# Performance work log

Hardware: AMD Instinct MI355X
Metric: run time of the kernel (lower is better)

## Reference

```python
import jax, jax.numpy as jnp
import numpy as np
from jax import lax

B, C, D, H, W = 2, 64, 16, 16, 16  # n = D*H*W = 4096; conv output length = n-2 = 4094
K = 3  # conv kernel size, dilation=2, padding=1


def setup_inputs() -> dict:
    key = jax.random.key(0)
    k1, k2, k3 = jax.random.split(key, 3)
    x = jax.random.normal(k1, (B, C, D, H, W), dtype=jnp.float32)
    # Conv1d params: weight [out_ch, in_ch, k], bias [out_ch]; PyTorch default init scale
    fan_in = C * K
    bound = 1.0 / np.sqrt(fan_in)
    conv_w = jax.random.uniform(k2, (C, C, K), jnp.float32, -bound, bound)
    conv_b = jax.random.uniform(k3, (C,), jnp.float32, -bound, bound)
    return {"x": x, "conv_w": conv_w, "conv_b": conv_b}


def _dspa(x, conv_w, conv_b):
    b, c, d, h, w = x.shape
    x1 = x.reshape(b, c, -1)  # [b, c, n]
    # dilated Conv1d: kernel=3, stride=1, padding=1, dilation=2 -> length n-2
    x2 = lax.conv_general_dilated(
        x1, conv_w,
        window_strides=(1,), padding=[(1, 1)], rhs_dilation=(2,),
        dimension_numbers=("NCH", "OIH", "NCH"),
    ) + conv_b[None, :, None]  # [b, c, n-2]
    # scores = bmm(x1^T, x2): [b, n, n-2]
    scores = jnp.einsum("bcn,bcm->bnm", x1, x2)
    # torch nn.Softmax() (dim=None) on a 3D tensor resolves to dim=0 (legacy behavior)
    x3 = jax.nn.softmax(scores, axis=0)  # [b, n, n-2]
    # x4 = bmm(x2, x3^T): [b, c, n]
    x4 = jnp.einsum("bcm,bnm->bcn", x2, x3)
    out = x1 + x4
    return out.reshape(b, c, d, h, w)


def reference(x, conv_w, conv_b):
    return _dspa(x, conv_w, conv_b)
```

## Files before the change

### kernel.cpp

```cpp
#include <hip/hip_runtime.h>

typedef unsigned short u16;
typedef unsigned int u32;
typedef __attribute__((ext_vector_type(8))) short bf16x8;
typedef __attribute__((ext_vector_type(4))) float f32x4;

#define NJ 4094

__device__ __forceinline__ u16 f2bf(float f) {
  union { float f; unsigned u; } v;
  v.f = f;
  unsigned r = v.u + 0x7fffu + ((v.u >> 16) & 1u);
  return (u16)(r >> 16);
}

__device__ __forceinline__ u32 pk_bf(float a, float b) {
  u32 ua = __float_as_uint(a) + 0x8000u;
  u32 ub = __float_as_uint(b) + 0x8000u;
  return __builtin_amdgcn_perm(ub, ua, 0x07060302u);
}

__global__ __launch_bounds__(256) void conv_kernel(
    const float* __restrict__ x, const float* __restrict__ w,
    const float* __restrict__ bias, u16* __restrict__ x2n, u16* __restrict__ x2T,
    float* __restrict__ out) {
  __shared__ float xs[64 * 68];
  __shared__ float wl[64 * 64 * 3];
  const int b = blockIdx.x >> 6, jt = blockIdx.x & 63;
  const int t = threadIdx.x;
  for (int idx = t; idx < 64 * 68; idx += 256) {
    int i = idx / 68, p = idx - i * 68;
    int jg = jt * 64 - 1 + p;
    float v = 0.f;
    if (jg >= 0 && jg < 4096) v = x[(b * 64 + i) * 4096 + jg];
    xs[idx] = v;
  }
  for (int idx = t; idx < 64 * 64 * 3; idx += 256) {
    int tap = idx % 3, ci = idx / 3;
    int c = ci >> 6, i = ci & 63;
    wl[(i * 64 + c) * 3 + tap] = w[idx];
  }
  __syncthreads();
  for (int idx = t; idx < 64 * 64; idx += 256) {
    int i = idx >> 6, k = idx & 63;
    out[(b * 64 + i) * 4096 + jt * 64 + k] = xs[i * 68 + k + 1];
  }
  const int c = t & 63, jsub = t >> 6;
  float acc[16];
  float bv = bias[c];
#pragma unroll
  for (int k = 0; k < 16; k++) acc[k] = bv;
  for (int i = 0; i < 64; i++) {
    float w0 = wl[(i * 64 + c) * 3 + 0];
    float w1 = wl[(i * 64 + c) * 3 + 1];
    float w2 = wl[(i * 64 + c) * 3 + 2];
    const float* xr = &xs[i * 68 + jsub * 16];
#pragma unroll
    for (int k = 0; k < 16; k++)
      acc[k] += w0 * xr[k] + w1 * xr[k + 2] + w2 * xr[k + 4];
  }
#pragma unroll
  for (int k = 0; k < 16; k++) {
    int jg = jt * 64 + jsub * 16 + k;
    float v = (jg < NJ) ? acc[k] : 0.f;
    u16 hv = f2bf(v);
    x2n[(b * 64 + c) * 4096 + jg] = hv;
    x2T[(b * 4096 + jg) * 64 + c] = hv;
  }
}

__global__ __launch_bounds__(256, 3) void fused_kernel(
    const float* __restrict__ x, const u16* __restrict__ x2n_g,
    const u16* __restrict__ x2T_g, float* __restrict__ out) {
  __shared__ u16 P[2][2 * 64 * 72];
  const int t = threadIdx.x;
  const int wave = t >> 6, lane = t & 63;
  const int q = lane >> 4, ln = lane & 15;
  const int i0 = blockIdx.x * 64;
  const int jc = blockIdx.y;

  u16* xs = P[1];
#pragma unroll
  for (int rep = 0; rep < 32; rep++) {
    int idx = rep * 256 + t;
    int il = idx & 63, c = (idx >> 6) & 63, b = idx >> 12;
    float v = x[(b * 64 + c) * 4096 + i0 + il];
    if (b) v = -v;
    xs[(b * 64 + il) * 72 + c] = f2bf(v);
  }
  __syncthreads();

  bf16x8 b1[2][4][2];
#pragma unroll
  for (int b = 0; b < 2; b++)
#pragma unroll
    for (int ist = 0; ist < 4; ist++)
#pragma unroll
      for (int kc = 0; kc < 2; kc++)
        b1[b][ist][kc] = *(const bf16x8*)&xs[(b * 64 + ist * 16 + ln) * 72 + kc * 32 + q * 8];

  f32x4 acc[2][4];
#pragma unroll
  for (int a = 0; a < 2; a++)
#pragma unroll
    for (int bq = 0; bq < 4; bq++) acc[a][bq] = (f32x4){0.f, 0.f, 0.f, 0.f};

  const int b2 = wave >> 1, cs2 = (wave & 1) * 2;

  for (int jt = jc * 4; jt < jc * 4 + 4; jt++) {
    const int j0 = jt * 64;
    u16* Ps = P[jt & 1];
    f32x4 ps[4];
#pragma unroll
    for (int ist = 0; ist < 4; ist++) ps[ist] = (f32x4){0.f, 0.f, 0.f, 0.f};
#pragma unroll
    for (int b = 0; b < 2; b++)
#pragma unroll
      for (int kc = 0; kc < 2; kc++) {
        bf16x8 af = *(const bf16x8*)&x2T_g[(b * 4096 + j0 + wave * 16 + ln) * 64 + kc * 32 + q * 8];
#pragma unroll
        for (int ist = 0; ist < 4; ist++)
          ps[ist] = __builtin_amdgcn_mfma_f32_16x16x32_bf16(af, b1[b][ist][kc], ps[ist], 0, 0, 0);
      }
#pragma unroll
    for (int ist = 0; ist < 4; ist++) {
      float p0[4], p1[4];
#pragma unroll
      for (int r = 0; r < 4; r++) {
        float e = __expf(-ps[ist][r]);
        p0[r] = __builtin_amdgcn_rcpf(1.f + e);
        p1[r] = 1.f - p0[r];
      }
      uint2 o0 = make_uint2(pk_bf(p0[0], p0[1]), pk_bf(p0[2], p0[3]));
      uint2 o1 = make_uint2(pk_bf(p1[0], p1[1]), pk_bf(p1[2], p1[3]));
      *(uint2*)&Ps[(0 + ist * 16 + ln) * 72 + wave * 16 + q * 4] = o0;
      *(uint2*)&Ps[(64 + ist * 16 + ln) * 72 + wave * 16 + q * 4] = o1;
    }
    __syncthreads();
#pragma unroll
    for (int kc = 0; kc < 2; kc++) {
      bf16x8 af2[2], pb[4];
#pragma unroll
      for (int cst = 0; cst < 2; cst++)
        af2[cst] = *(const bf16x8*)&x2n_g[(b2 * 64 + (cs2 + cst) * 16 + ln) * 4096 + j0 + kc * 32 + q * 8];
#pragma unroll
      for (int ist = 0; ist < 4; ist++)
        pb[ist] = *(const bf16x8*)&Ps[(b2 * 64 + ist * 16 + ln) * 72 + kc * 32 + q * 8];
#pragma unroll
      for (int cst = 0; cst < 2; cst++)
#pragma unroll
        for (int ist = 0; ist < 4; ist++)
          acc[cst][ist] =
              __builtin_amdgcn_mfma_f32_16x16x32_bf16(af2[cst], pb[ist], acc[cst][ist], 0, 0, 0);
    }
  }
#pragma unroll
  for (int cst = 0; cst < 2; cst++)
#pragma unroll
    for (int ist = 0; ist < 4; ist++)
#pragma unroll
      for (int r = 0; r < 4; r++) {
        int c = (cs2 + cst) * 16 + q * 4 + r;
        int ii = i0 + ist * 16 + ln;
        unsafeAtomicAdd(&out[(b2 * 64 + c) * 4096 + ii], acc[cst][ist][r]);
      }
}

extern "C" void kernel_launch(void* const* d_in, const int* in_sizes, int n_in,
                              void* d_out, int out_size, void* d_ws, size_t ws_size,
                              hipStream_t stream) {
  const float* x = (const float*)d_in[0];
  const float* w = (const float*)d_in[1];
  const float* bias = (const float*)d_in[2];
  float* out = (float*)d_out;
  u16* x2n = (u16*)d_ws;
  u16* x2T = x2n + 2 * 64 * 4096;

  conv_kernel<<<128, 256, 0, stream>>>(x, w, bias, x2n, x2T, out);
  dim3 grid(64, 16);
  fused_kernel<<<grid, 256, 0, stream>>>(x, x2n, x2T, out);
}
```

Before: 118.4 us.

## Replace atomic accumulation with per-chunk partial buffers and a reduction kernel

Each fused block now writes its partial sums to a dedicated slice of a workspace buffer instead of doing float atomics into the output. A new reduce kernel adds the residual x and the 16 partials with float4 loads. The conv kernel skips writing x into out on this path, and the launch bound of the fused kernel is raised to 4 waves per SIMD. The change removes atomic contention, but it adds a third launch and about 8 MB of extra partial traffic, and it falls back to the atomic path if the workspace is too small.

```diff
diff --git a/kernel.cpp b/kernel.cpp
--- a/kernel.cpp
+++ b/kernel.cpp
@@ -20,6 +20,7 @@
   return __builtin_amdgcn_perm(ub, ua, 0x07060302u);
 }
 
+template <bool WRITE_OUT>
 __global__ __launch_bounds__(256) void conv_kernel(
     const float* __restrict__ x, const float* __restrict__ w,
     const float* __restrict__ bias, u16* __restrict__ x2n, u16* __restrict__ x2T,
@@ -41,9 +42,11 @@
     wl[(i * 64 + c) * 3 + tap] = w[idx];
   }
   __syncthreads();
-  for (int idx = t; idx < 64 * 64; idx += 256) {
-    int i = idx >> 6, k = idx & 63;
-    out[(b * 64 + i) * 4096 + jt * 64 + k] = xs[i * 68 + k + 1];
+  if (WRITE_OUT) {
+    for (int idx = t; idx < 64 * 64; idx += 256) {
+      int i = idx >> 6, k = idx & 63;
+      out[(b * 64 + i) * 4096 + jt * 64 + k] = xs[i * 68 + k + 1];
+    }
   }
   const int c = t & 63, jsub = t >> 6;
   float acc[16];
@@ -69,9 +72,11 @@
   }
 }
 
-__global__ __launch_bounds__(256, 3) void fused_kernel(
+template <bool ATOMIC>
+__global__ __launch_bounds__(256, 4) void fused_kernel(
     const float* __restrict__ x, const u16* __restrict__ x2n_g,
-    const u16* __restrict__ x2T_g, float* __restrict__ out) {
+    const u16* __restrict__ x2T_g, float* __restrict__ part_g,
+    float* __restrict__ out) {
   __shared__ u16 P[2][2 * 64 * 72];
   const int t = threadIdx.x;
   const int wave = t >> 6, lane = t & 63;
@@ -162,8 +167,25 @@
       for (int r = 0; r < 4; r++) {
         int c = (cs2 + cst) * 16 + q * 4 + r;
         int ii = i0 + ist * 16 + ln;
-        unsafeAtomicAdd(&out[(b2 * 64 + c) * 4096 + ii], acc[cst][ist][r]);
+        if (ATOMIC) {
+          unsafeAtomicAdd(&out[(b2 * 64 + c) * 4096 + ii], acc[cst][ist][r]);
+        } else {
+          part_g[(((jc * 2 + b2) * 64 + c) << 12) + ii] = acc[cst][ist][r];
+        }
       }
+}
+
+__global__ __launch_bounds__(256) void reduce_kernel(
+    const float4* __restrict__ x, const float4* __restrict__ part,
+    float4* __restrict__ out) {
+  int i = blockIdx.x * 256 + threadIdx.x;
+  float4 s = x[i];
+#pragma unroll
+  for (int jc = 0; jc < 16; jc++) {
+    float4 p = part[jc * 131072 + i];
+    s.x += p.x; s.y += p.y; s.z += p.z; s.w += p.w;
+  }
+  out[i] = s;
 }
 
 extern "C" void kernel_launch(void* const* d_in, const int* in_sizes, int n_in,
@@ -175,8 +197,16 @@
   float* out = (float*)d_out;
   u16* x2n = (u16*)d_ws;
   u16* x2T = x2n + 2 * 64 * 4096;
-
-  conv_kernel<<<128, 256, 0, stream>>>(x, w, bias, x2n, x2T, out);
+  float* part = (float*)(x2T + 2 * 64 * 4096);
+
+  const size_t need = 2u * 64 * 4096 * 2 * 2 + 16u * 2 * 64 * 4096 * 4;
   dim3 grid(64, 16);
-  fused_kernel<<<grid, 256, 0, stream>>>(x, x2n, x2T, out);
-}
+  if (ws_size >= need) {
+    conv_kernel<false><<<128, 256, 0, stream>>>(x, w, bias, x2n, x2T, out);
+    fused_kernel<false><<<grid, 256, 0, stream>>>(x, x2n, x2T, part, out);
+    reduce_kernel<<<512, 256, 0, stream>>>((const float4*)x, (const float4*)part, (float4*)out);
+  } else {
+    conv_kernel<true><<<128, 256, 0, stream>>>(x, w, bias, x2n, x2T, out);
+    fused_kernel<true><<<grid, 256, 0, stream>>>(x, x2n, x2T, nullptr, out);
+  }
+}
```

Result: faster. 113.0 us (-4.6%).
